# Kernel optimization log

Hardware: AMD Instinct MI355X
Metric: run time of the kernel (lower is better)

Reference implementation:

```python
import jax, jax.numpy as jnp
import numpy as np

B, MAXLEN, PE, N, EMB, VOCAB = 16, 1024, 256, 1024, 256, 8000
GO_OUT, NODE_F, C, HID, K, EPS = 64, 64, 128, 64, 3, 1e-5


def _bn_feat(x, g, b):  # BatchNorm1d on [B, F], batch stats (training mode)
    m = x.mean(axis=0, keepdims=True)
    v = x.var(axis=0, keepdims=True)
    return (x - m) * jax.lax.rsqrt(v + EPS) * g + b


def _bn_node(x, g, b):  # BatchNorm1d on [B, N, C] with channel axis = node axis (1)
    m = x.mean(axis=(0, 2), keepdims=True)
    v = x.var(axis=(0, 2), keepdims=True)
    return (x - m) * jax.lax.rsqrt(v + EPS) * g[None, :, None] + b[None, :, None]


def setup_inputs() -> dict:
    key = jax.random.key(0)
    ks = jax.random.split(key, 10)
    d = {}
    d["data"] = jax.random.randint(ks[0], (B, MAXLEN + PE), 0, VOCAB)
    d["node_features"] = jax.random.normal(ks[1], (N, NODE_F), jnp.float32)
    d["go_adj"] = jax.random.uniform(ks[2], (N, N), jnp.float32)
    d["batch_adj"] = jnp.zeros((1,), jnp.int32)
    d["emb_table"] = jax.random.normal(ks[3], (VOCAB, EMB), jnp.float32) * 0.02
    d["w_go"] = jax.random.normal(ks[4], (2 * PE, N * GO_OUT), jnp.float32) * 0.02
    d["b_go"] = jnp.zeros((N * GO_OUT,), jnp.float32)
    d["wq"] = jax.random.normal(ks[5], (C, HID), jnp.float32) * 0.1
    d["wk"] = jax.random.normal(ks[6], (C, HID), jnp.float32) * 0.1
    d["theta"] = jax.random.normal(ks[7], (K, C, C), jnp.float32) * 0.05
    d["g1"] = jnp.ones((2 * PE,), jnp.float32); d["b1"] = jnp.zeros((2 * PE,), jnp.float32)
    d["g3"] = jnp.ones((N,), jnp.float32); d["b3"] = jnp.zeros((N,), jnp.float32)
    d["g4"] = jnp.ones((N,), jnp.float32); d["b4"] = jnp.zeros((N,), jnp.float32)
    d["w_out"] = jax.random.normal(ks[8], (C, 1), jnp.float32) * 0.1
    d["b_out"] = jnp.zeros((1,), jnp.float32)
    return d


def reference(data, node_features, go_adj, batch_adj, emb_table, w_go, b_go,
              wq, wk, theta, g1, b1, g3, b3, g4, b4, w_out, b_out):
    # PositionalEncoding(outfea=1, len=256): pe = sin(arange(256))
    pe = jnp.sin(jnp.arange(PE, dtype=jnp.float32))
    inp1 = data[:, :MAXLEN]                       # [B, MAXLEN] token ids
    inp2 = data[:, MAXLEN:].astype(jnp.float32)   # [B, 256] dense features
    # FeatureModel: embedding + mean-pool over sequence -> [B, 256]
    feat = jnp.take(emb_table, inp1, axis=0).mean(axis=1) + pe
    inp2 = inp2 + pe
    m1 = _bn_feat(jnp.concatenate([feat, inp2], axis=1), g1, b1)   # [B, 512]
    # GoFeature: per-class feature projection -> [B, N, GO_OUT]
    go = jax.nn.relu(m1 @ w_go + b_go).reshape(B, N, GO_OUT)
    nf = jnp.broadcast_to(node_features[None], (B, N, NODE_F))
    x = jnp.concatenate([go, nf], axis=2)                          # [B, N, C]
    x = _bn_node(x, g3, b3)
    # FunctionAttention: scaled dot-product scores over nodes -> [B, N, N]
    q = jnp.einsum('bnc,ch->bnh', x, wq)
    kk = jnp.einsum('bnc,ch->bnh', x, wk)
    att = jnp.einsum('bnh,bmh->bnm', q, kk) / jnp.sqrt(jnp.float32(HID))
    adj = go_adj[None] + jax.nn.softmax(att, axis=1)               # [B, N, N]
    # FunctionConv: K-hop Chebyshev recurrence on batched adjacency
    t_prev, t_cur = x, jnp.einsum('bnm,bmc->bnc', adj, x)
    out = jnp.einsum('bnc,cd->bnd', t_prev, theta[0]) + jnp.einsum('bnc,cd->bnd', t_cur, theta[1])
    for i in range(2, K):
        t_next = 2.0 * jnp.einsum('bnm,bmc->bnc', adj, t_cur) - t_prev
        out = out + jnp.einsum('bnc,cd->bnd', t_next, theta[i])
        t_prev, t_cur = t_cur, t_next
    x2 = _bn_node(out + x, g4, b4)
    x2 = jax.nn.relu(x2)  # dropout omitted for deterministic reference
    return (x2 @ w_out + b_out)[..., 0]          # [B, N]
```

## Files before the change

### kernel.cpp

```cpp
#include <hip/hip_runtime.h>

namespace {
constexpr int kB = 16;
constexpr int kMAXLEN = 1024;
constexpr int kPE = 256;
constexpr int kN = 1024;
constexpr int kEMB = 256;
constexpr int kC = 128;
constexpr float kEPS = 1e-5f;

constexpr size_t OFF_FEATPART = 0;
constexpr size_t OFF_M1       = 262144;
constexpr size_t OFF_X        = 270336;
constexpr size_t OFF_Z        = OFF_X    + 2097152;
constexpr size_t OFF_TCUR     = OFF_Z    + 2097152;
constexpr size_t OFF_TNEXT    = OFF_TCUR + 2097152;
constexpr size_t OFF_GOPART   = OFF_TNEXT+ 2097152;
constexpr size_t OFF_PSUM     = OFF_GOPART + 4194304;
constexpr size_t OFF_SUMZ     = OFF_PSUM + 262144;
constexpr size_t OFF_SUMZZ    = OFF_SUMZ + 16384;
constexpr size_t OFF_ADJ      = OFF_SUMZZ + 16384;
constexpr size_t OFF_XT       = OFF_ADJ  + 8388608;
constexpr size_t OFF_Q        = OFF_XT   + 1048576;
constexpr size_t OFF_K        = OFF_Q    + 524288;
constexpr size_t OFF_TT       = OFF_K    + 524288;

typedef __attribute__((ext_vector_type(8))) short bfrag;
typedef __attribute__((ext_vector_type(4))) float f32x4;

__device__ inline ushort f2bf(float f) {
  unsigned u = __float_as_uint(f);
  unsigned r = (u + 0x7FFFu + ((u >> 16) & 1u)) >> 16;
  return (ushort)r;
}
}

__global__ __launch_bounds__(256) void k_embsum(const int* __restrict__ data,
                                                const float* __restrict__ emb,
                                                float* __restrict__ featpart) {
  const int b = blockIdx.x, ch = blockIdx.y;
  const int e = threadIdx.x;
  const int* row = data + b * (kMAXLEN + kPE) + ch * 16;
  float acc = 0.f;
#pragma unroll 4
  for (int l = 0; l < 16; ++l) {
    acc += emb[(size_t)row[l] * kEMB + e];
  }
  featpart[((b * 64 + ch) << 8) + e] = acc;
}

__global__ __launch_bounds__(256) void k_bn_feat(const float* __restrict__ featpart,
                                                 const int* __restrict__ data,
                                                 const float* __restrict__ g1,
                                                 const float* __restrict__ b1,
                                                 float* __restrict__ m1t) {
  const int tid = threadIdx.x;
  const int jl = tid >> 3, part = tid & 7;
  const int j = blockIdx.x * 32 + jl;
  float v[kB];
  if (j < kPE) {
#pragma unroll
    for (int b = 0; b < kB; ++b) {
      float s = 0.f;
      const int ch0 = part * 8;
#pragma unroll
      for (int ch = 0; ch < 8; ++ch)
        s += featpart[((b * 64 + ch0 + ch) << 8) + j];
      v[b] = s;
    }
  } else {
#pragma unroll
    for (int b = 0; b < kB; ++b)
      v[b] = (part == 0) ? (float)data[b * (kMAXLEN + kPE) + kMAXLEN + (j - kPE)] : 0.f;
  }
#pragma unroll
  for (int m = 1; m < 8; m <<= 1) {
#pragma unroll
    for (int b = 0; b < kB; ++b) v[b] += __shfl_xor(v[b], m);
  }
  const float pe = (j < kPE) ? sinf((float)j) : sinf((float)(j - kPE));
#pragma unroll
  for (int b = 0; b < kB; ++b)
    v[b] = (j < kPE) ? (v[b] * (1.f / 1024.f) + pe) : (v[b] + pe);
  float s = 0.f;
#pragma unroll
  for (int b = 0; b < kB; ++b) s += v[b];
  const float mean = s * (1.f / kB);
  float s2 = 0.f;
#pragma unroll
  for (int b = 0; b < kB; ++b) { float d = v[b] - mean; s2 += d * d; }
  const float inv = rsqrtf(s2 * (1.f / kB) + kEPS);
  if (part == 0) {
    const float g = g1[j], bb = b1[j];
    float o[kB];
#pragma unroll
    for (int b = 0; b < kB; ++b) o[b] = (v[b] - mean) * inv * g + bb;
#pragma unroll
    for (int q = 0; q < 4; ++q)
      *reinterpret_cast<float4*>(&m1t[j * kB + q * 4]) =
          *reinterpret_cast<float4*>(&o[q * 4]);
  }
}

__global__ __launch_bounds__(256) void k_go_gemm2(const float* __restrict__ m1t,
                                                  const float* __restrict__ w_go,
                                                  float* __restrict__ part) {
  const int c0 = blockIdx.x * 1024 + threadIdx.x * 4;
  const int k0 = blockIdx.y * 128;
  float4 acc[kB];
#pragma unroll
  for (int b = 0; b < kB; ++b) acc[b] = make_float4(0.f, 0.f, 0.f, 0.f);
#pragma unroll 4
  for (int k = 0; k < 128; ++k) {
    const float4 w = *reinterpret_cast<const float4*>(&w_go[(size_t)(k0 + k) * 65536 + c0]);
    const float* mrow = m1t + (size_t)(k0 + k) * kB;
#pragma unroll
    for (int b = 0; b < kB; ++b) {
      const float m = mrow[b];
      acc[b].x += m * w.x; acc[b].y += m * w.y;
      acc[b].z += m * w.z; acc[b].w += m * w.w;
    }
  }
  const size_t kb16 = (size_t)blockIdx.y * kB;
#pragma unroll
  for (int b = 0; b < kB; ++b) {
    *reinterpret_cast<float4*>(&part[(kb16 + b) * 65536 + c0]) = acc[b];
  }
}

__global__ __launch_bounds__(256) void k_go_bn(const float* __restrict__ part,
                                               const float* __restrict__ b_go,
                                               const float* __restrict__ nf,
                                               const float* __restrict__ g3,
                                               const float* __restrict__ b3,
                                               float* __restrict__ x) {
  const int n = blockIdx.x;
  const int tid = threadIdx.x;
  __shared__ float nfs[64];
  if (tid < 64) nfs[tid] = nf[n * 64 + tid];
  float val[4];
  float s = 0.f, s2 = 0.f;
#pragma unroll
  for (int i = 0; i < 4; ++i) {
    const int e = i * 256 + tid;
    const int b = e >> 6, c = e & 63;
    float a = part[(size_t)b * 65536 + n * 64 + c];
#pragma unroll
    for (int kb = 1; kb < 4; ++kb)
      a += part[(size_t)(kb * kB + b) * 65536 + n * 64 + c];
    a = fmaxf(a + b_go[n * 64 + c], 0.f);
    val[i] = a;
    s += a; s2 += a * a;
  }
  __syncthreads();
  if (tid < 64) {
    const float v = nfs[tid];
    s += 16.f * v; s2 += 16.f * v * v;
  }
  for (int o = 32; o > 0; o >>= 1) { s += __shfl_down(s, o); s2 += __shfl_down(s2, o); }
  __shared__ float ls[4], ls2[4];
  __shared__ float sscale, sshift;
  const int w = tid >> 6;
  if ((tid & 63) == 0) { ls[w] = s; ls2[w] = s2; }
  __syncthreads();
  if (tid == 0) {
    float S = ls[0] + ls[1] + ls[2] + ls[3];
    float S2 = ls2[0] + ls2[1] + ls2[2] + ls2[3];
    float mean = S * (1.f / 2048.f);
    float var = fmaxf(S2 * (1.f / 2048.f) - mean * mean, 0.f);
    float inv = rsqrtf(var + kEPS);
    float gg = g3[n];
    sscale = inv * gg;
    sshift = b3[n] - mean * inv * gg;
  }
  __syncthreads();
  const float scale = sscale, shift = sshift;
#pragma unroll
  for (int i = 0; i < 4; ++i) {
    const int e = i * 256 + tid;
    const int b = e >> 6, c = e & 63;
    x[((size_t)(b * kN + n)) * kC + c] = val[i] * scale + shift;
  }
#pragma unroll
  for (int i = 0; i < 4; ++i) {
    const int e = i * 256 + tid;
    const int b = e >> 6, c = e & 63;
    x[((size_t)(b * kN + n)) * kC + 64 + c] = nfs[c] * scale + shift;
  }
}

__global__ __launch_bounds__(256) void k_qkgen(const float* __restrict__ x,
                                               const float* __restrict__ wq,
                                               const float* __restrict__ wk,
                                               ushort* __restrict__ qb,
                                               ushort* __restrict__ kb,
                                               ushort* __restrict__ xt) {
  __shared__ float a_s[32 * 68];
  __shared__ float w_s[32 * 128];
  const int row0 = blockIdx.x * 32;
  const int bb = row0 >> 10, n0 = row0 & 1023;
  const int tid = threadIdx.x;
  const int tr = tid >> 5, tc = tid & 31;
  const int r0 = tr * 4, c0 = tc * 4;
  float acc[4][4] = {};
  for (int kc = 0; kc < 4; ++kc) {
    const int k0 = kc * 32;
    __syncthreads();
    {
      int r = tid >> 3, kk4 = tid & 7;
      float4 v = *reinterpret_cast<const float4*>(&x[(size_t)(row0 + r) * kC + k0 + kk4 * 4]);
      *reinterpret_cast<float4*>(&a_s[r * 68 + kk4 * 4]) = v;
    }
    for (int it = 0; it < 16; ++it) {
      int e = it * 256 + tid;
      int kk = e >> 7, h2 = e & 127;
      int c = k0 + kk;
      float v = (h2 < 64) ? wq[c * 64 + h2] : wk[c * 64 + (h2 - 64)];
      w_s[kk * 128 + h2] = v;
    }
    __syncthreads();
#pragma unroll
    for (int q = 0; q < 4; ++q) {
      const int e = q * 256 + tid;
      const int kk = e >> 5, r = e & 31;
      xt[(size_t)(bb * kC + k0 + kk) * kN + n0 + r] = f2bf(a_s[r * 68 + kk]);
    }
#pragma unroll 8
    for (int k = 0; k < 32; ++k) {
      float a[4];
#pragma unroll
      for (int i = 0; i < 4; ++i) a[i] = a_s[(r0 + i) * 68 + k];
      float4 b4 = *reinterpret_cast<float4*>(&w_s[k * 128 + c0]);
      float bj[4] = {b4.x, b4.y, b4.z, b4.w};
#pragma unroll
      for (int i = 0; i < 4; ++i)
#pragma unroll
        for (int j = 0; j < 4; ++j) acc[i][j] += a[i] * bj[j];
    }
  }
  const bool isq = (c0 < 64);
  const int h0 = isq ? c0 : (c0 - 64);
  ushort* oh = isq ? qb : kb;
#pragma unroll
  for (int i = 0; i < 4; ++i) {
    ushort hs[4];
#pragma unroll
    for (int j = 0; j < 4; ++j) hs[j] = f2bf(acc[i][j]);
    const size_t o = (size_t)(row0 + r0 + i) * 64 + h0;
    *reinterpret_cast<ushort4*>(&oh[o]) = *reinterpret_cast<ushort4*>(hs);
  }
}

__global__ __launch_bounds__(512) void k_att_stats(const ushort* __restrict__ qb,
                                                   const ushort* __restrict__ kb,
                                                   float* __restrict__ psum) {
  const int nt = blockIdx.x, b = blockIdx.y;
  const int mc0 = blockIdx.z * 4;
  __shared__ uint4 smem4[2560];
  char* smem = (char*)smem4;
  const int tid = threadIdx.x;
  const int lane = tid & 63, w = tid >> 6;
  const int l15 = lane & 15, lg = lane >> 4;

  {
    const int r = tid >> 3, ch = tid & 7;
    const size_t g = (size_t)(b * kN + nt * 64 + r) * 64 + ch * 8;
    const unsigned off = (unsigned)(r * 128 + ch * 16) ^ (unsigned)((r & 7) << 4);
    *reinterpret_cast<uint4*>(smem + off) = *reinterpret_cast<const uint4*>(qb + g);
  }

  const int c0s = tid >> 3, c1s = 64 + (tid >> 3);
  const int chs = tid & 7;
  const unsigned offK0 = (unsigned)(c0s * 128 + chs * 16) ^ (unsigned)((c0s & 7) << 4);
  const unsigned offK1 = (unsigned)(c1s * 128 + chs * 16) ^ (unsigned)((c1s & 7) << 4);
  const size_t gK0 = (size_t)(b * kN + mc0 * 128 + c0s) * 64 + chs * 8;
  const size_t gK1 = (size_t)(b * kN + mc0 * 128 + c1s) * 64 + chs * 8;

  uint4 ph0 = *reinterpret_cast<const uint4*>(kb + gK0);
  uint4 ph1 = *reinterpret_cast<const uint4*>(kb + gK1);
  *reinterpret_cast<uint4*>(smem + 8192 + offK0) = ph0;
  *reinterpret_cast<uint4*>(smem + 8192 + offK1) = ph1;
  {
    const size_t k1 = (size_t)128 * 64;
    ph0 = *reinterpret_cast<const uint4*>(kb + gK0 + k1);
    ph1 = *reinterpret_cast<const uint4*>(kb + gK1 + k1);
  }
  __syncthreads();

  for (int it = 0; it < 4; ++it) {
    const int mc = mc0 + it;
    const unsigned bufC = 8192 + (unsigned)(it & 1) * 16384;
    const unsigned bufN = 8192 + (unsigned)((it + 1) & 1) * 16384;
    if (it < 3) {
      *reinterpret_cast<uint4*>(smem + bufN + offK0) = ph0;
      *reinterpret_cast<uint4*>(smem + bufN + offK1) = ph1;
      if (it < 2) {
        const size_t k2 = (size_t)(it + 2) * 128 * 64;
        ph0 = *reinterpret_cast<const uint4*>(kb + gK0 + k2);
        ph1 = *reinterpret_cast<const uint4*>(kb + gK1 + k2);
      }
    }
    f32x4 acc[4] = {{0.f,0.f,0.f,0.f},{0.f,0.f,0.f,0.f},{0.f,0.f,0.f,0.f},{0.f,0.f,0.f,0.f}};
#pragma unroll
    for (int ss = 0; ss < 2; ++ss) {
      const int r = w * 16 + l15;
      const unsigned aoff = ((unsigned)(r * 128 + ss * 64 + lg * 16) ^ (unsigned)((r & 7) << 4)) + bufC;
      bfrag ah = *reinterpret_cast<const bfrag*>(smem + aoff);
#pragma unroll
      for (int nf = 0; nf < 4; ++nf) {
        const int c = nf * 16 + l15;
        const unsigned boff = (unsigned)(c * 128 + ss * 64 + lg * 16) ^ (unsigned)((c & 7) << 4);
        bfrag bh = *reinterpret_cast<const bfrag*>(smem + boff);
        acc[nf] = __builtin_amdgcn_mfma_f32_16x16x32_bf16(ah, bh, acc[nf], 0, 0, 0);
      }
    }
#pragma unroll
    for (int i = 0; i < 4; ++i) {
      float sm = __expf(acc[0][i] * 0.125f) + __expf(acc[1][i] * 0.125f)
               + __expf(acc[2][i] * 0.125f) + __expf(acc[3][i] * 0.125f);
#pragma unroll
      for (int msk = 1; msk < 16; msk <<= 1) sm += __shfl_xor(sm, msk);
      if (l15 == 0) {
        const int m = mc * 128 + w * 16 + lg * 4 + i;
        psum[(size_t)(b * 16 + nt) * kN + m] = sm;
      }
    }
    __syncthreads();
  }
}

__global__ __launch_bounds__(512) void k_adj_emit(const ushort* __restrict__ qb,
                                                  const ushort* __restrict__ kb,
                                                  const float* __restrict__ go_adj,
                                                  const float* __restrict__ psum,
                                                  ushort* __restrict__ adj) {
  const int mc = blockIdx.x, nt = blockIdx.y, b = blockIdx.z;
  __shared__ uint4 smem4[2304];
  __shared__ float cinvs[128];
  char* smem = (char*)smem4;
  float* c32 = (float*)smem4;
  const int tid = threadIdx.x;
  const int lane = tid & 63, w = tid >> 6;
  const int wr = w >> 2, wc = w & 3;
  const int l15 = lane & 15, lg = lane >> 4;

  if (tid < 128) {
    const int m = mc * 128 + tid;
    float S = 0.f;
#pragma unroll
    for (int c = 0; c < 16; ++c) S += psum[(size_t)(b * 16 + c) * kN + m];
    cinvs[tid] = 1.f / S;
  }
  {
    const int r = tid >> 3, ch = tid & 7;
    const size_t g = (size_t)(b * kN + nt * 64 + r) * 64 + ch * 8;
    const unsigned off = (unsigned)(r * 128 + ch * 16) ^ (unsigned)((r & 7) << 4);
    *reinterpret_cast<uint4*>(smem + off) = *reinterpret_cast<const uint4*>(qb + g);
  }
#pragma unroll
  for (int p = 0; p < 2; ++p) {
    const int e = p * 512 + tid;
    const int c = e >> 3, ch = e & 7;
    const size_t g = (size_t)(b * kN + mc * 128 + c) * 64 + ch * 8;
    const unsigned off = (unsigned)(c * 128 + ch * 16) ^ (unsigned)((c & 7) << 4);
    *reinterpret_cast<uint4*>(smem + 8192 + off) = *reinterpret_cast<const uint4*>(kb + g);
  }
  __syncthreads();
  f32x4 acc[2][2] = {{{0.f,0.f,0.f,0.f},{0.f,0.f,0.f,0.f}},
                     {{0.f,0.f,0.f,0.f},{0.f,0.f,0.f,0.f}}};
#pragma unroll
  for (int ss = 0; ss < 2; ++ss) {
    bfrag ah[2], bh[2];
#pragma unroll
    for (int nf = 0; nf < 2; ++nf) {
      const int r = wr * 32 + nf * 16 + l15;
      const unsigned aoff = (unsigned)(r * 128 + ss * 64 + lg * 16) ^ (unsigned)((r & 7) << 4);
      ah[nf] = *reinterpret_cast<const bfrag*>(smem + aoff);
    }
#pragma unroll
    for (int mf = 0; mf < 2; ++mf) {
      const int c = wc * 32 + mf * 16 + l15;
      const unsigned boff = (unsigned)(c * 128 + ss * 64 + lg * 16) ^ (unsigned)((c & 7) << 4);
      bh[mf] = *reinterpret_cast<const bfrag*>(smem + 8192 + boff);
    }
#pragma unroll
    for (int nf = 0; nf < 2; ++nf)
#pragma unroll
      for (int mf = 0; mf < 2; ++mf)
        acc[nf][mf] = __builtin_amdgcn_mfma_f32_16x16x32_bf16(ah[nf], bh[mf], acc[nf][mf], 0, 0, 0);
  }
  __syncthreads();
#pragma unroll
  for (int mf = 0; mf < 2; ++mf) {
    const int mLoc = wc * 32 + mf * 16 + l15;
    const float I = cinvs[mLoc];
#pragma unroll
    for (int nf = 0; nf < 2; ++nf) {
#pragma unroll
      for (int i = 0; i < 4; ++i) {
        const int nLoc = wr * 32 + nf * 16 + lg * 4 + i;
        c32[nLoc * 132 + mLoc] = __expf(acc[nf][mf][i] * 0.125f) * I;
      }
    }
  }
  __syncthreads();
#pragma unroll
  for (int p = 0; p < 2; ++p) {
    const int e = p * 512 + tid;
    const int n = e >> 4, m0 = (e & 15) * 8;
    const float* cr = &c32[n * 132 + m0];
    const float* ga = &go_adj[(size_t)(nt * 64 + n) * kN + mc * 128 + m0];
    ushort hs[8];
#pragma unroll
    for (int j = 0; j < 8; ++j) hs[j] = f2bf(cr[j] + ga[j]);
    const size_t o = (size_t)(b * kN + nt * 64 + n) * kN + mc * 128 + m0;
    *reinterpret_cast<uint4*>(&adj[o]) = *reinterpret_cast<uint4*>(hs);
  }
}

__global__ __launch_bounds__(512) void k_adjmm_mfma(const ushort* __restrict__ adj,
                                                    const ushort* __restrict__ xt,
                                                    const float* __restrict__ Zsub,
                                                    float* __restrict__ Y, float alpha,
                                                    ushort* __restrict__ yt) {
  const int bid = blockIdx.x;
  const int swz = (bid & 7) * 32 + (bid >> 3);
  const int b = swz >> 4, rb = swz & 15;
  __shared__ uint4 smem4[3072];
  char* smem = (char*)smem4;
  float* c32 = (float*)smem4;
  const int tid = threadIdx.x;
  const int lane = tid & 63, w = tid >> 6;
  const int wr = w >> 1, wc = w & 1;
  const int l15 = lane & 15, lg = lane >> 4;

  const int ra = tid >> 3, cha = tid & 7;
  const unsigned offA = (unsigned)(ra * 128 + cha * 16) ^ (unsigned)((ra & 7) << 4);
  const size_t gA = ((size_t)(b * kN + rb * 64 + ra)) * kN + cha * 8;
  const int cb0 = tid >> 3, cb1 = 64 + (tid >> 3);
  const unsigned offB0 = (unsigned)(cb0 * 128 + cha * 16) ^ (unsigned)((cb0 & 7) << 4);
  const unsigned offB1 = (unsigned)(cb1 * 128 + cha * 16) ^ (unsigned)((cb1 & 7) << 4);
  const size_t gB0 = ((size_t)b * kC + cb0) * kN + cha * 8;
  const size_t gB1 = ((size_t)b * kC + cb1) * kN + cha * 8;

  f32x4 acc[4] = {{0.f,0.f,0.f,0.f},{0.f,0.f,0.f,0.f},{0.f,0.f,0.f,0.f},{0.f,0.f,0.f,0.f}};

  uint4 pa  = *reinterpret_cast<const uint4*>(adj + gA);
  uint4 pb0 = *reinterpret_cast<const uint4*>(xt + gB0);
  uint4 pb1 = *reinterpret_cast<const uint4*>(xt + gB1);
  *reinterpret_cast<uint4*>(smem + offA)         = pa;
  *reinterpret_cast<uint4*>(smem + 8192 + offB0) = pb0;
  *reinterpret_cast<uint4*>(smem + 8192 + offB1) = pb1;
  pa  = *reinterpret_cast<const uint4*>(adj + gA + 64);
  pb0 = *reinterpret_cast<const uint4*>(xt + gB0 + 64);
  pb1 = *reinterpret_cast<const uint4*>(xt + gB1 + 64);
  __syncthreads();

  for (int kt = 0; kt < 16; ++kt) {
    const unsigned bufC = (unsigned)(kt & 1) * 24576;
    const unsigned bufN = (unsigned)((kt + 1) & 1) * 24576;
    if (kt < 15) {
      *reinterpret_cast<uint4*>(smem + bufN + offA)         = pa;
      *reinterpret_cast<uint4*>(smem + bufN + 8192 + offB0) = pb0;
      *reinterpret_cast<uint4*>(smem + bufN + 8192 + offB1) = pb1;
      if (kt < 14) {
        const int k2 = (kt + 2) * 64;
        pa  = *reinterpret_cast<const uint4*>(adj + gA + k2);
        pb0 = *reinterpret_cast<const uint4*>(xt + gB0 + k2);
        pb1 = *reinterpret_cast<const uint4*>(xt + gB1 + k2);
      }
    }
#pragma unroll
    for (int ss = 0; ss < 2; ++ss) {
      const int r = wr * 16 + l15;
      const unsigned aoff = ((unsigned)(r * 128 + ss * 64 + lg * 16) ^ (unsigned)((r & 7) << 4)) + bufC;
      bfrag ah = *reinterpret_cast<const bfrag*>(smem + aoff);
      bfrag bh[4];
#pragma unroll
      for (int ct = 0; ct < 4; ++ct) {
        const int c = wc * 64 + ct * 16 + l15;
        const unsigned boff = ((unsigned)(c * 128 + ss * 64 + lg * 16) ^ (unsigned)((c & 7) << 4)) + bufC;
        bh[ct] = *reinterpret_cast<const bfrag*>(smem + 8192 + boff);
      }
#pragma unroll
      for (int ct = 0; ct < 4; ++ct)
        acc[ct] = __builtin_amdgcn_mfma_f32_16x16x32_bf16(ah, bh[ct], acc[ct], 0, 0, 0);
    }
    __syncthreads();
  }
  const int orow = rb * 64 + wr * 16 + lg * 4;
#pragma unroll
  for (int ct = 0; ct < 4; ++ct) {
    const int ocol = wc * 64 + ct * 16 + l15;
#pragma unroll
    for (int i = 0; i < 4; ++i) {
      const size_t idx = ((size_t)(b * kN + orow + i)) * kC + ocol;
      float v = alpha * acc[ct][i];
      if (Zsub) v -= Zsub[idx];
      Y[idx] = v;
      if (yt) c32[(wr * 16 + lg * 4 + i) * 132 + ocol] = v;
    }
  }
  if (yt) {
    __syncthreads();
    const int c = tid >> 2, nch = tid & 3;
    const int n0 = nch * 16;
    ushort hs[16];
#pragma unroll
    for (int j = 0; j < 16; ++j) hs[j] = f2bf(c32[(n0 + j) * 132 + c]);
    const size_t obase = (size_t)(b * kC + c) * kN + rb * 64 + n0;
    *reinterpret_cast<uint4*>(&yt[obase]) = *reinterpret_cast<uint4*>(hs);
    *reinterpret_cast<uint4*>(&yt[obase + 8]) = *reinterpret_cast<uint4*>(hs + 8);
  }
}

__global__ __launch_bounds__(256) void k_theta(const float* __restrict__ x,
                                               const float* __restrict__ tcur,
                                               const float* __restrict__ tnext,
                                               const float* __restrict__ theta,
                                               float* __restrict__ z,
                                               float* __restrict__ sumz,
                                               float* __restrict__ sumzz) {
  __shared__ float a_s[32 * 68];
  __shared__ float w_s[32 * 128];
  const int row0 = blockIdx.x * 32;
  const int tid = threadIdx.x;
  const int tr = tid >> 5, tc = tid & 31;
  const int r0 = tr * 4, c0 = tc * 4;
  float acc[4][4] = {};
  const float* srcs[3] = {x, tcur, tnext};
  for (int s = 0; s < 3; ++s) {
    const float* A = srcs[s];
    for (int kc = 0; kc < 4; ++kc) {
      const int k0 = kc * 32;
      __syncthreads();
      {
        int r = tid >> 3, kk4 = tid & 7;
        float4 v = *reinterpret_cast<const float4*>(&A[(size_t)(row0 + r) * kC + k0 + kk4 * 4]);
        *reinterpret_cast<float4*>(&a_s[r * 68 + kk4 * 4]) = v;
      }
#pragma unroll
      for (int it = 0; it < 4; ++it) {
        int e4 = it * 256 + tid;
        int kk = e4 >> 5, d4 = e4 & 31;
        float4 v = *reinterpret_cast<const float4*>(
            &theta[(size_t)s * 16384 + (size_t)(k0 + kk) * kC + d4 * 4]);
        *reinterpret_cast<float4*>(&w_s[kk * 128 + d4 * 4]) = v;
      }
      __syncthreads();
#pragma unroll 8
      for (int k = 0; k < 32; ++k) {
        float a[4];
#pragma unroll
        for (int i = 0; i < 4; ++i) a[i] = a_s[(r0 + i) * 68 + k];
        float4 b4 = *reinterpret_cast<float4*>(&w_s[k * 128 + c0]);
        float bj[4] = {b4.x, b4.y, b4.z, b4.w};
#pragma unroll
        for (int i = 0; i < 4; ++i)
#pragma unroll
          for (int j = 0; j < 4; ++j) acc[i][j] += a[i] * bj[j];
      }
    }
  }
  float rs[4], rq[4];
#pragma unroll
  for (int i = 0; i < 4; ++i) {
    size_t idx = (size_t)(row0 + r0 + i) * kC + c0;
    float4 xv = *reinterpret_cast<const float4*>(&x[idx]);
    float4 o = {acc[i][0] + xv.x, acc[i][1] + xv.y, acc[i][2] + xv.z, acc[i][3] + xv.w};
    *reinterpret_cast<float4*>(&z[idx]) = o;
    rs[i] = o.x + o.y + o.z + o.w;
    rq[i] = o.x * o.x + o.y * o.y + o.z * o.z + o.w * o.w;
  }
#pragma unroll
  for (int m = 1; m < 32; m <<= 1) {
#pragma unroll
    for (int i = 0; i < 4; ++i) { rs[i] += __shfl_xor(rs[i], m); rq[i] += __shfl_xor(rq[i], m); }
  }
  if (tc == 0) {
#pragma unroll
    for (int i = 0; i < 4; ++i) {
      sumz[row0 + r0 + i] = rs[i];
      sumzz[row0 + r0 + i] = rq[i];
    }
  }
}

__global__ __launch_bounds__(256) void k_final(const float* __restrict__ z,
                                               const float* __restrict__ sumz,
                                               const float* __restrict__ sumzz,
                                               const float* __restrict__ g4,
                                               const float* __restrict__ b4v,
                                               const float* __restrict__ w_out,
                                               const float* __restrict__ b_out,
                                               float* __restrict__ out) {
  const int n = blockIdx.x;
  const int tid = threadIdx.x;
  __shared__ float sscale, sshift;
  if (tid < 16) {
    float a = sumz[tid * kN + n];
    float q = sumzz[tid * kN + n];
#pragma unroll
    for (int m = 1; m < 16; m <<= 1) { a += __shfl_xor(a, m); q += __shfl_xor(q, m); }
    if (tid == 0) {
      float mean = a * (1.f / 2048.f);
      float var = fmaxf(q * (1.f / 2048.f) - mean * mean, 0.f);
      float inv = rsqrtf(var + kEPS);
      float gg = g4[n];
      sscale = inv * gg;
      sshift = b4v[n] - mean * inv * gg;
    }
  }
  __syncthreads();
  const float scale = sscale, shift = sshift;
  const int b = tid >> 4, c0 = (tid & 15) * 8;
  float p = 0.f;
#pragma unroll
  for (int j = 0; j < 8; ++j) {
    float v = z[(size_t)(b * kN + n) * kC + c0 + j] * scale + shift;
    v = fmaxf(v, 0.f);
    p += v * w_out[c0 + j];
  }
  for (int o = 8; o > 0; o >>= 1) p += __shfl_down(p, o, 16);
  if ((tid & 15) == 0) out[b * kN + n] = p + b_out[0];
}

extern "C" void kernel_launch(void* const* d_in, const int* in_sizes, int n_in,
                              void* d_out, int out_size, void* d_ws, size_t ws_size,
                              hipStream_t stream) {
  const int*   data = (const int*)d_in[0];
  const float* node_features = (const float*)d_in[1];
  const float* go_adj = (const float*)d_in[2];
  const float* emb  = (const float*)d_in[4];
  const float* w_go = (const float*)d_in[5];
  const float* b_go = (const float*)d_in[6];
  const float* wq   = (const float*)d_in[7];
  const float* wk   = (const float*)d_in[8];
  const float* theta= (const float*)d_in[9];
  const float* g1   = (const float*)d_in[10];
  const float* b1   = (const float*)d_in[11];
  const float* g3   = (const float*)d_in[12];
  const float* b3   = (const float*)d_in[13];
  const float* g4   = (const float*)d_in[14];
  const float* b4   = (const float*)d_in[15];
  const float* w_out= (const float*)d_in[16];
  const float* b_out= (const float*)d_in[17];

  float* ws = (float*)d_ws;
  float* featpart = ws + OFF_FEATPART;
  float* m1t   = ws + OFF_M1;
  float* x     = ws + OFF_X;
  float* z     = ws + OFF_Z;
  float* tcur  = ws + OFF_TCUR;
  float* tnext = ws + OFF_TNEXT;
  float* gopart= ws + OFF_GOPART;
  float* psum  = ws + OFF_PSUM;
  float* sumz  = ws + OFF_SUMZ;
  float* sumzz = ws + OFF_SUMZZ;
  ushort* adj  = (ushort*)(ws + OFF_ADJ);
  ushort* xt   = (ushort*)(ws + OFF_XT);
  ushort* qb   = (ushort*)(ws + OFF_Q);
  ushort* kb   = (ushort*)(ws + OFF_K);
  ushort* tt   = (ushort*)(ws + OFF_TT);

  k_embsum<<<dim3(16, 64), 256, 0, stream>>>(data, emb, featpart);
  k_bn_feat<<<16, 256, 0, stream>>>(featpart, data, g1, b1, m1t);
  k_go_gemm2<<<dim3(64, 4), 256, 0, stream>>>(m1t, w_go, gopart);
  k_go_bn<<<1024, 256, 0, stream>>>(gopart, b_go, node_features, g3, b3, x);
  k_qkgen<<<512, 256, 0, stream>>>(x, wq, wk, qb, kb, xt);
  k_att_stats<<<dim3(16, 16, 2), 512, 0, stream>>>(qb, kb, psum);
  k_adj_emit<<<dim3(8, 16, 16), 512, 0, stream>>>(qb, kb, go_adj, psum, adj);
  k_adjmm_mfma<<<256, 512, 0, stream>>>(adj, xt, nullptr, tcur, 1.0f, tt);
  k_adjmm_mfma<<<256, 512, 0, stream>>>(adj, tt, x, tnext, 2.0f, nullptr);
  k_theta<<<512, 256, 0, stream>>>(x, tcur, tnext, theta, z, sumz, sumzz);
  k_final<<<1024, 256, 0, stream>>>(z, sumz, sumzz, g4, b4, w_out, b_out, (float*)d_out);
}
```

Before: 173.7 us.

## Run theta projection on bf16 MFMA with pre-transposed bf16 theta

Replaces the scalar fp32 shared-memory GEMM that applies the three Chebyshev theta matrices with a bf16 MFMA kernel. Each wave converts its fp32 activation rows to bf16 on the fly. Theta is transposed and converted to bf16 once, inside the existing feature-BN kernel, so the B fragments can be loaded directly from global memory. Row sums and sums of squares for the final BatchNorm are now reduced through shared memory across two column waves. This trades fp32 accuracy in the projection for bf16 rounding.

```diff
diff --git a/kernel.cpp b/kernel.cpp
--- a/kernel.cpp
+++ b/kernel.cpp
@@ -24,6 +24,7 @@
 constexpr size_t OFF_Q        = OFF_XT   + 1048576;
 constexpr size_t OFF_K        = OFF_Q    + 524288;
 constexpr size_t OFF_TT       = OFF_K    + 524288;
+constexpr size_t OFF_THT      = OFF_TT   + 1048576;
 
 typedef __attribute__((ext_vector_type(8))) short bfrag;
 typedef __attribute__((ext_vector_type(4))) float f32x4;
@@ -53,8 +54,20 @@
                                                  const int* __restrict__ data,
                                                  const float* __restrict__ g1,
                                                  const float* __restrict__ b1,
-                                                 float* __restrict__ m1t) {
-  const int tid = threadIdx.x;
+                                                 const float* __restrict__ theta,
+                                                 float* __restrict__ m1t,
+                                                 ushort* __restrict__ thT) {
+  const int tid = threadIdx.x;
+  {
+    const int gid = blockIdx.x * 256 + tid;
+#pragma unroll
+    for (int j = 0; j < 12; ++j) {
+      const int idx = gid * 12 + j;
+      const int s = idx >> 14, rem = idx & 16383;
+      const int d = rem >> 7, c = rem & 127;
+      thT[idx] = f2bf(theta[(size_t)(s * 128 + c) * 128 + d]);
+    }
+  }
   const int jl = tid >> 3, part = tid & 7;
   const int j = blockIdx.x * 32 + jl;
   float v[kB];
@@ -514,75 +527,72 @@
   }
 }
 
-__global__ __launch_bounds__(256) void k_theta(const float* __restrict__ x,
-                                               const float* __restrict__ tcur,
-                                               const float* __restrict__ tnext,
-                                               const float* __restrict__ theta,
-                                               float* __restrict__ z,
-                                               float* __restrict__ sumz,
-                                               float* __restrict__ sumzz) {
-  __shared__ float a_s[32 * 68];
-  __shared__ float w_s[32 * 128];
-  const int row0 = blockIdx.x * 32;
-  const int tid = threadIdx.x;
-  const int tr = tid >> 5, tc = tid & 31;
-  const int r0 = tr * 4, c0 = tc * 4;
-  float acc[4][4] = {};
+__global__ __launch_bounds__(512) void k_theta_mfma(const float* __restrict__ x,
+                                                    const float* __restrict__ tcur,
+                                                    const float* __restrict__ tnext,
+                                                    const ushort* __restrict__ thT,
+                                                    float* __restrict__ z,
+                                                    float* __restrict__ sumz,
+                                                    float* __restrict__ sumzz) {
+  const int rb = blockIdx.x, b = blockIdx.y;
+  const int tid = threadIdx.x;
+  const int lane = tid & 63, w = tid >> 6;
+  const int wr = w >> 1, wc = w & 1;
+  const int l15 = lane & 15, lg = lane >> 4;
+  __shared__ float rsS[2][64], rqS[2][64];
+
+  f32x4 acc[4] = {{0.f,0.f,0.f,0.f},{0.f,0.f,0.f,0.f},{0.f,0.f,0.f,0.f},{0.f,0.f,0.f,0.f}};
   const float* srcs[3] = {x, tcur, tnext};
+  const size_t arow = ((size_t)(b * kN + rb * 64 + wr * 16 + l15)) * kC;
   for (int s = 0; s < 3; ++s) {
-    const float* A = srcs[s];
-    for (int kc = 0; kc < 4; ++kc) {
-      const int k0 = kc * 32;
-      __syncthreads();
-      {
-        int r = tid >> 3, kk4 = tid & 7;
-        float4 v = *reinterpret_cast<const float4*>(&A[(size_t)(row0 + r) * kC + k0 + kk4 * 4]);
-        *reinterpret_cast<float4*>(&a_s[r * 68 + kk4 * 4]) = v;
+    const float* A = srcs[s] + arow;
+    const ushort* TH = thT + (size_t)s * 16384;
+#pragma unroll
+    for (int ss = 0; ss < 4; ++ss) {
+      const int k0 = ss * 32 + lg * 8;
+      float4 a0 = *reinterpret_cast<const float4*>(A + k0);
+      float4 a1 = *reinterpret_cast<const float4*>(A + k0 + 4);
+      ushort av[8] = {f2bf(a0.x), f2bf(a0.y), f2bf(a0.z), f2bf(a0.w),
+                      f2bf(a1.x), f2bf(a1.y), f2bf(a1.z), f2bf(a1.w)};
+      bfrag af = *reinterpret_cast<bfrag*>(av);
+#pragma unroll
+      for (int ct = 0; ct < 4; ++ct) {
+        const int d = wc * 64 + ct * 16 + l15;
+        bfrag bf = *reinterpret_cast<const bfrag*>(TH + (size_t)d * 128 + k0);
+        acc[ct] = __builtin_amdgcn_mfma_f32_16x16x32_bf16(af, bf, acc[ct], 0, 0, 0);
       }
-#pragma unroll
-      for (int it = 0; it < 4; ++it) {
-        int e4 = it * 256 + tid;
-        int kk = e4 >> 5, d4 = e4 & 31;
-        float4 v = *reinterpret_cast<const float4*>(
-            &theta[(size_t)s * 16384 + (size_t)(k0 + kk) * kC + d4 * 4]);
-        *reinterpret_cast<float4*>(&w_s[kk * 128 + d4 * 4]) = v;
-      }
-      __syncthreads();
-#pragma unroll 8
-      for (int k = 0; k < 32; ++k) {
-        float a[4];
-#pragma unroll
-        for (int i = 0; i < 4; ++i) a[i] = a_s[(r0 + i) * 68 + k];
-        float4 b4 = *reinterpret_cast<float4*>(&w_s[k * 128 + c0]);
-        float bj[4] = {b4.x, b4.y, b4.z, b4.w};
-#pragma unroll
-        for (int i = 0; i < 4; ++i)
-#pragma unroll
-          for (int j = 0; j < 4; ++j) acc[i][j] += a[i] * bj[j];
-      }
-    }
-  }
-  float rs[4], rq[4];
-#pragma unroll
-  for (int i = 0; i < 4; ++i) {
-    size_t idx = (size_t)(row0 + r0 + i) * kC + c0;
-    float4 xv = *reinterpret_cast<const float4*>(&x[idx]);
-    float4 o = {acc[i][0] + xv.x, acc[i][1] + xv.y, acc[i][2] + xv.z, acc[i][3] + xv.w};
-    *reinterpret_cast<float4*>(&z[idx]) = o;
-    rs[i] = o.x + o.y + o.z + o.w;
-    rq[i] = o.x * o.x + o.y * o.y + o.z * o.z + o.w * o.w;
-  }
-#pragma unroll
-  for (int m = 1; m < 32; m <<= 1) {
+    }
+  }
+  float rs[4] = {0.f, 0.f, 0.f, 0.f}, rq[4] = {0.f, 0.f, 0.f, 0.f};
+  const int nBase = rb * 64 + wr * 16 + lg * 4;
+#pragma unroll
+  for (int ct = 0; ct < 4; ++ct) {
+    const int ocol = wc * 64 + ct * 16 + l15;
+#pragma unroll
+    for (int i = 0; i < 4; ++i) {
+      const size_t idx = ((size_t)(b * kN + nBase + i)) * kC + ocol;
+      float v = acc[ct][i] + x[idx];
+      z[idx] = v;
+      rs[i] += v; rq[i] += v * v;
+    }
+  }
+#pragma unroll
+  for (int m = 1; m < 16; m <<= 1) {
 #pragma unroll
     for (int i = 0; i < 4; ++i) { rs[i] += __shfl_xor(rs[i], m); rq[i] += __shfl_xor(rq[i], m); }
   }
-  if (tc == 0) {
+  if (l15 == 0) {
 #pragma unroll
     for (int i = 0; i < 4; ++i) {
-      sumz[row0 + r0 + i] = rs[i];
-      sumzz[row0 + r0 + i] = rq[i];
-    }
+      rsS[wc][wr * 16 + lg * 4 + i] = rs[i];
+      rqS[wc][wr * 16 + lg * 4 + i] = rq[i];
+    }
+  }
+  __syncthreads();
+  if (tid < 64) {
+    const int n = rb * 64 + tid;
+    sumz[(size_t)b * kN + n] = rsS[0][tid] + rsS[1][tid];
+    sumzz[(size_t)b * kN + n] = rqS[0][tid] + rqS[1][tid];
   }
 }
 
@@ -662,9 +672,10 @@
   ushort* qb   = (ushort*)(ws + OFF_Q);
   ushort* kb   = (ushort*)(ws + OFF_K);
   ushort* tt   = (ushort*)(ws + OFF_TT);
+  ushort* thT  = (ushort*)(ws + OFF_THT);
 
   k_embsum<<<dim3(16, 64), 256, 0, stream>>>(data, emb, featpart);
-  k_bn_feat<<<16, 256, 0, stream>>>(featpart, data, g1, b1, m1t);
+  k_bn_feat<<<16, 256, 0, stream>>>(featpart, data, g1, b1, theta, m1t, thT);
   k_go_gemm2<<<dim3(64, 4), 256, 0, stream>>>(m1t, w_go, gopart);
   k_go_bn<<<1024, 256, 0, stream>>>(gopart, b_go, node_features, g3, b3, x);
   k_qkgen<<<512, 256, 0, stream>>>(x, wq, wk, qb, kb, xt);
@@ -672,6 +683,6 @@
   k_adj_emit<<<dim3(8, 16, 16), 512, 0, stream>>>(qb, kb, go_adj, psum, adj);
   k_adjmm_mfma<<<256, 512, 0, stream>>>(adj, xt, nullptr, tcur, 1.0f, tt);
   k_adjmm_mfma<<<256, 512, 0, stream>>>(adj, tt, x, tnext, 2.0f, nullptr);
-  k_theta<<<512, 256, 0, stream>>>(x, tcur, tnext, theta, z, sumz, sumzz);
+  k_theta_mfma<<<dim3(16, 16), 512, 0, stream>>>(x, tcur, tnext, thT, z, sumz, sumzz);
   k_final<<<1024, 256, 0, stream>>>(z, sumz, sumzz, g4, b4, w_out, b_out, (float*)d_out);
 }
```

Result: faster. 166.3 us (-4.3%).
